# Kernel optimization log

Hardware: AMD Instinct MI355X
Metric: run time of the kernel (lower is better)

Reference implementation:

```python
import jax, jax.numpy as jnp
import numpy as np

B, C, D, H, W = 4, 64, 32, 64, 64
S, NH = 8, 4
HD = C // NH


def setup_inputs() -> dict:
    key = jax.random.key(0)
    ks = jax.random.split(key, 8)
    sc = 0.05
    return {
        "x": jax.random.normal(ks[0], (B, C, D, H, W), jnp.float32),
        "slot_init": jax.random.normal(ks[1], (1, C, S), jnp.float32),
        "slot_proj_w": jax.random.normal(ks[2], (C, C), jnp.float32) * sc,
        "slot_proj_b": jnp.zeros((C,), jnp.float32),
        "ln_g": jnp.ones((C,), jnp.float32),
        "ln_b": jnp.zeros((C,), jnp.float32),
        "in_proj_w": jax.random.normal(ks[3], (3 * C, C), jnp.float32) * sc,
        "in_proj_b": jnp.zeros((3 * C,), jnp.float32),
        "out_proj_w": jax.random.normal(ks[4], (C, C), jnp.float32) * sc,
        "out_proj_b": jnp.zeros((C,), jnp.float32),
        "feat_w": jax.random.normal(ks[5], (C, C), jnp.float32) * sc,
        "feat_b": jnp.zeros((C,), jnp.float32),
        "s2f_w": jax.random.normal(ks[6], (C, C), jnp.float32) * sc,
        "s2f_b": jnp.zeros((C,), jnp.float32),
    }


def _l2norm(v, axis):
    # F.normalize: v / max(||v||, eps)
    n = jnp.sqrt(jnp.sum(v * v, axis=axis, keepdims=True))
    return v / jnp.maximum(n, 1e-12)


def reference(x, slot_init, slot_proj_w, slot_proj_b, ln_g, ln_b,
              in_proj_w, in_proj_b, out_proj_w, out_proj_b,
              feat_w, feat_b, s2f_w, s2f_b):
    b, c, d, h, w = x.shape
    n = d * h * w
    x_flat = x.reshape(b, c, n)                                  # (b,c,N)
    slots = jnp.broadcast_to(slot_init, (b, c, S))               # (b,c,S)

    # ---- slot update: cosine-sim cross attention over N ----
    x_norm = _l2norm(x_flat, 1)
    slots_norm = _l2norm(slots, 1)
    sim = jnp.einsum('bcs,bcn->bsn', slots_norm, x_norm)         # (b,S,N)
    attn = jax.nn.softmax(sim, axis=2)
    updates = jnp.einsum('bcn,bsn->bsc', x_flat, attn)           # (b,S,c)
    slots_t = updates @ slot_proj_w.T + slot_proj_b              # (b,S,c)

    # ---- LayerNorm(channels) then tiny MHSA over S=8 slots ----
    mu = jnp.mean(slots_t, axis=-1, keepdims=True)
    var = jnp.mean((slots_t - mu) ** 2, axis=-1, keepdims=True)
    sn = (slots_t - mu) / jnp.sqrt(var + 1e-5) * ln_g + ln_b     # (b,S,c)

    qkv = sn @ in_proj_w.T + in_proj_b                           # (b,S,3c)
    q, k, v = jnp.split(qkv, 3, axis=-1)
    def heads(t):
        return t.reshape(b, S, NH, HD).transpose(0, 2, 1, 3)     # (b,H,S,hd)
    q, k, v = heads(q), heads(k), heads(v)
    scores = jnp.einsum('bhqd,bhkd->bhqk', q, k) / jnp.sqrt(jnp.float32(HD))
    a = jax.nn.softmax(scores, axis=-1)
    o = jnp.einsum('bhqk,bhkd->bhqd', a, v).transpose(0, 2, 1, 3).reshape(b, S, c)
    o = o @ out_proj_w.T + out_proj_b
    slots_t = slots_t + o                                        # (b,S,c)

    # ---- feature broadcast: 1x1x1 conv + slot->feature attention ----
    feat_flat = jnp.einsum('oc,bcn->bon', feat_w, x_flat) + feat_b[None, :, None]
    slots_feat = slots_t @ s2f_w.T + s2f_b                       # (b,S,c)
    sim2 = jnp.einsum('bsc,bcn->bsn', slots_feat, feat_flat)
    attn2 = jax.nn.softmax(sim2, axis=1)                         # softmax over slots
    out = jnp.einsum('bsc,bsn->bcn', slots_t, attn2)             # (b,c,N)
    return out.reshape(b, c, d, h, w) + x
```

## Files before the change

### kernel.cpp

```cpp
#include <hip/hip_runtime.h>
#include <hip/hip_bf16.h>

#define BB   4
#define CC   64
#define SS   8
#define NN   (32*64*64)
#define NH_  4
#define HD_  16
#define TN   256

typedef __attribute__((ext_vector_type(8))) short bf16x8;
typedef __attribute__((ext_vector_type(4))) float f32x4;

__device__ __forceinline__ unsigned short f2b(float f) {
    union { float f; unsigned u; } v; v.f = f;
    unsigned r = v.u + 0x7FFFu + ((v.u >> 16) & 1u);
    return (unsigned short)(r >> 16);
}

__global__ __launch_bounds__(256) void k_precomp(
    const float* __restrict__ slot_init,
    const float* __restrict__ s2fw, const float* __restrict__ s2fb,
    const float* __restrict__ fw, const float* __restrict__ fb,
    float* __restrict__ M, float* __restrict__ g0v,
    float* __restrict__ hv, float* __restrict__ h0,
    float* __restrict__ snT_ws)
{
    const int tid = threadIdx.x;
    if (blockIdx.x < 16) {
        const int cp = blockIdx.x*4 + (tid >> 6);
        const int c  = tid & 63;
        float acc = 0.f;
        #pragma unroll 8
        for (int o = 0; o < CC; ++o)
            acc += s2fw[o*CC + cp] * fw[o*CC + c];
        M[cp*CC + c] = acc;
    } else if (blockIdx.x == 16) {
        if (tid < 64) {
            float acc = 0.f;
            #pragma unroll 8
            for (int o = 0; o < CC; ++o) acc += s2fb[o] * fw[o*CC + tid];
            g0v[tid] = acc;
        } else if (tid < 128) {
            const int cp = tid - 64;
            float acc = 0.f;
            #pragma unroll 8
            for (int o = 0; o < CC; ++o) acc += s2fw[o*CC + cp] * fb[o];
            hv[cp] = acc;
        } else if (tid == 128) {
            float acc = 0.f;
            for (int o = 0; o < CC; ++o) acc += s2fb[o] * fb[o];
            *h0 = acc;
        }
    } else {
        __shared__ float nrm[SS];
        if (tid < 64) {
            const int s = tid & 7, ch = tid >> 3;
            float p = 0.f;
            #pragma unroll
            for (int j = 0; j < 8; ++j) {
                float v = slot_init[(ch*8 + j)*SS + s];
                p += v*v;
            }
            p += __shfl_xor(p, 8); p += __shfl_xor(p, 16); p += __shfl_xor(p, 32);
            if (tid < 8) nrm[s] = fmaxf(sqrtf(p), 1e-12f);
        }
        __syncthreads();
        for (int i = tid; i < SS*CC; i += 256) {
            const int s = i >> 6, c = i & 63;
            snT_ws[i] = slot_init[c*SS + s] / nrm[s];
        }
    }
}

__global__ __launch_bounds__(256, 4) void k_slots_attn(
    const float* __restrict__ x, const float* __restrict__ snT_ws,
    float* __restrict__ U_part, float* __restrict__ sume_part, int bpb)
{
    __shared__ short xt[CC * TN];
    __shared__ short et[9 * TN];
    __shared__ float snT[SS * CC];

    const int tid = threadIdx.x;
    const int b   = blockIdx.x / bpb;
    const int blk = blockIdx.x % bpb;

    if (tid < 64) *(int2*)&et[8*TN + tid*4] = make_int2(0, 0);
    if (tid < 128) *(float4*)&snT[tid*4] = *(const float4*)&snT_ws[tid*4];

    const int lane = tid & 63, wv = tid >> 6;
    const int n7 = tid & 7, nq3 = tid >> 3;
    f32x4 accU = {0.f, 0.f, 0.f, 0.f};
    float accS[SS];
    #pragma unroll
    for (int s = 0; s < SS; ++s) accS[s] = 0.f;

    const float* xb = x + (size_t)b * CC * NN;
    const int ntiles = NN / TN;

    for (int t = blk; t < ntiles; t += bpb) {
        const int n0 = t * TN;

        float xc[CC];
        #pragma unroll
        for (int c = 0; c < CC; ++c) xc[c] = xb[(size_t)c * NN + n0 + tid];

        __syncthreads();

        #pragma unroll
        for (int c = 0; c < CC; ++c)
            xt[c*TN + (((nq3 ^ (c & 7)) << 3) | n7)] = (short)f2b(xc[c]);

        {
            float ss = 0.f;
            float a[SS];
            #pragma unroll
            for (int s = 0; s < SS; ++s) a[s] = 0.f;
            #pragma unroll
            for (int c4 = 0; c4 < 16; ++c4) {
                const float xv0 = xc[c4*4+0], xv1 = xc[c4*4+1];
                const float xv2 = xc[c4*4+2], xv3 = xc[c4*4+3];
                ss += xv0*xv0 + xv1*xv1 + xv2*xv2 + xv3*xv3;
                #pragma unroll
                for (int s = 0; s < SS; ++s) {
                    const float4 g4 = *(const float4*)&snT[s*CC + c4*4];
                    a[s] += g4.x*xv0 + g4.y*xv1 + g4.z*xv2 + g4.w*xv3;
                }
            }
            const float invn = 1.f / fmaxf(sqrtf(ss), 1e-12f);
            #pragma unroll
            for (int s = 0; s < SS; ++s) {
                const float e = __expf(a[s] * invn);
                accS[s] += e;
                et[s*TN + (((nq3 ^ s) << 3) | n7)] = (short)f2b(e);
            }
        }
        __syncthreads();

        {
            const int ca  = (wv << 4) + (lane & 15);
            const int rbq = lane & 15;
            const int rb  = (rbq < 8) ? rbq : 8;
            const int p   = lane >> 4;
            #pragma unroll
            for (int k = 0; k < TN/32; ++k) {
                const int sa = ((((k << 2) + p) ^ (lane & 7)) << 3);
                bf16x8 af  = *(const bf16x8*)&xt[ca*TN + sa];
                bf16x8 bfr = *(const bf16x8*)&et[rb*TN + sa];
                accU = __builtin_amdgcn_mfma_f32_16x16x32_bf16(af, bfr, accU, 0, 0, 0);
            }
        }
    }
    __syncthreads();

    {
        const size_t base = ((size_t)(b*bpb + blk) * SS) * CC;
        if ((lane & 15) < SS) {
            const int s  = lane & 15;
            const int c0 = (wv << 4) + ((lane >> 4) << 2);
            #pragma unroll
            for (int r = 0; r < 4; ++r)
                U_part[base + s*CC + c0 + r] = accU[r];
        }
    }
    {
        float* red = (float*)xt;
        #pragma unroll
        for (int s = 0; s < SS; ++s) red[s*256 + tid] = accS[s];
        __syncthreads();
        const int s = tid >> 5, j = tid & 31;
        float v = 0.f;
        #pragma unroll
        for (int k = 0; k < 8; ++k) v += red[s*256 + j*8 + k];
        v += __shfl_xor(v, 1); v += __shfl_xor(v, 2); v += __shfl_xor(v, 4);
        v += __shfl_xor(v, 8); v += __shfl_xor(v, 16);
        if (j == 0) sume_part[(size_t)(b*bpb + blk)*SS + s] = v;
    }
}

__global__ __launch_bounds__(256) void k_reduce2(
    const float* __restrict__ U_part, const float* __restrict__ sume_part,
    float* __restrict__ upd_g, int bpb)
{
    __shared__ float part[4][64];
    __shared__ float lbuf[256];
    __shared__ float Lsh;
    const int tid = threadIdx.x;
    const int b = blockIdx.x >> 3, s = blockIdx.x & 7;
    const int c = tid & 63, kc = tid >> 6;
    const int cnt = bpb >> 2;

    float lv = 0.f;
    for (int k = tid; k < bpb; k += 256)
        lv += sume_part[(size_t)(b*bpb + k)*SS + s];
    lbuf[tid] = lv;

    float acc[8];
    #pragma unroll
    for (int j = 0; j < 8; ++j) acc[j] = 0.f;
    const float* base = U_part + ((size_t)(b*bpb + kc*cnt)*SS + s)*CC + c;
    for (int k = 0; k < cnt; k += 8) {
        #pragma unroll
        for (int j = 0; j < 8; ++j)
            acc[j] += base[(size_t)(k + j) * SS * CC];
    }
    part[kc][c] = ((acc[0]+acc[1]) + (acc[2]+acc[3]))
                + ((acc[4]+acc[5]) + (acc[6]+acc[7]));
    __syncthreads();

    if (tid < 128) lbuf[tid] += lbuf[tid + 128];
    __syncthreads();
    if (tid < 64) {
        float v = lbuf[tid] + lbuf[tid + 64];
        v += __shfl_xor(v, 1); v += __shfl_xor(v, 2); v += __shfl_xor(v, 4);
        v += __shfl_xor(v, 8); v += __shfl_xor(v, 16); v += __shfl_xor(v, 32);
        if (tid == 0) Lsh = v;
    }
    __syncthreads();

    if (tid < 64) {
        float u = part[0][c] + part[1][c] + part[2][c] + part[3][c];
        upd_g[((size_t)b*SS + s)*CC + c] = u / Lsh;
    }
}

__global__ __launch_bounds__(256) void k_slots_small(
    const float* __restrict__ upd_g,
    const float* __restrict__ spw, const float* __restrict__ spb,
    const float* __restrict__ lng, const float* __restrict__ lnb,
    const float* __restrict__ ipw, const float* __restrict__ ipb,
    const float* __restrict__ opw, const float* __restrict__ opb,
    const float* __restrict__ M, const float* __restrict__ g0v,
    const float* __restrict__ hv, const float* __restrict__ h0,
    float* __restrict__ st_out, float* __restrict__ g_out, float* __restrict__ h_out)
{
    __shared__ float upd[SS*CC];
    __shared__ float st [SS*CC];
    __shared__ float snb[SS*CC];
    __shared__ float qkv[SS*3*CC];
    __shared__ float ot [SS*CC];

    const int tid  = threadIdx.x;
    const int b    = blockIdx.x;
    const int c    = tid & 63;
    const int quad = tid >> 6;
    const int r0 = quad*2, r1 = r0 + 1;
    float wreg[CC];

    #pragma unroll
    for (int i = 0; i < 16; ++i)
        *(float4*)&wreg[i*4] = *(const float4*)(spw + c*CC + i*4);
    upd[r0*CC + c] = upd_g[(b*SS + r0)*CC + c];
    upd[r1*CC + c] = upd_g[(b*SS + r1)*CC + c];
    __syncthreads();

    {
        const float bias = spb[c];
        float a0 = bias, a1 = bias;
        #pragma unroll
        for (int i = 0; i < 16; ++i) {
            float4 u0 = *(const float4*)&upd[r0*CC + i*4];
            float4 u1 = *(const float4*)&upd[r1*CC + i*4];
            a0 += u0.x*wreg[i*4+0] + u0.y*wreg[i*4+1] + u0.z*wreg[i*4+2] + u0.w*wreg[i*4+3];
            a1 += u1.x*wreg[i*4+0] + u1.y*wreg[i*4+1] + u1.z*wreg[i*4+2] + u1.w*wreg[i*4+3];
        }
        st[r0*CC + c] = a0;
        st[r1*CC + c] = a1;
    }
    __syncthreads();

    {
        const int row = tid >> 5, l = tid & 31;
        float v0 = st[row*CC + l], v1 = st[row*CC + l + 32];
        float sum = v0 + v1;
        sum += __shfl_xor(sum, 1); sum += __shfl_xor(sum, 2); sum += __shfl_xor(sum, 4);
        sum += __shfl_xor(sum, 8); sum += __shfl_xor(sum, 16);
        const float mu = sum * (1.f/64.f);
        const float d0 = v0 - mu, d1 = v1 - mu;
        float vs = d0*d0 + d1*d1;
        vs += __shfl_xor(vs, 1); vs += __shfl_xor(vs, 2); vs += __shfl_xor(vs, 4);
        vs += __shfl_xor(vs, 8); vs += __shfl_xor(vs, 16);
        const float rstd = rsqrtf(vs * (1.f/64.f) + 1e-5f);
        snb[row*CC + l]      = d0 * rstd * lng[l]      + lnb[l];
        snb[row*CC + l + 32] = d1 * rstd * lng[l + 32] + lnb[l + 32];
    }
    __syncthreads();

    for (int m = 0; m < 3; ++m) {
        #pragma unroll
        for (int i = 0; i < 16; ++i)
            *(float4*)&wreg[i*4] = *(const float4*)(ipw + (size_t)(m*CC + c)*CC + i*4);
        const float bias = ipb[m*CC + c];
        float a0 = bias, a1 = bias;
        #pragma unroll
        for (int i = 0; i < 16; ++i) {
            float4 u0 = *(const float4*)&snb[r0*CC + i*4];
            float4 u1 = *(const float4*)&snb[r1*CC + i*4];
            a0 += u0.x*wreg[i*4+0] + u0.y*wreg[i*4+1] + u0.z*wreg[i*4+2] + u0.w*wreg[i*4+3];
            a1 += u1.x*wreg[i*4+0] + u1.y*wreg[i*4+1] + u1.z*wreg[i*4+2] + u1.w*wreg[i*4+3];
        }
        qkv[r0*3*CC + m*CC + c] = a0;
        qkv[r1*3*CC + m*CC + c] = a1;
    }
    __syncthreads();

    if (tid < NH_*SS) {
        const int h = tid >> 3, q = tid & 7;
        float qreg[HD_];
        #pragma unroll
        for (int i = 0; i < 4; ++i)
            *(float4*)&qreg[i*4] = *(const float4*)&qkv[q*3*CC + h*HD_ + i*4];
        float srow[SS];
        float mx = -1e30f;
        #pragma unroll
        for (int k = 0; k < SS; ++k) {
            float acc = 0.f;
            #pragma unroll
            for (int d = 0; d < HD_; ++d)
                acc += qreg[d] * qkv[k*3*CC + CC + h*HD_ + d];
            srow[k] = acc * 0.25f;
            mx = fmaxf(mx, srow[k]);
        }
        float l = 0.f;
        #pragma unroll
        for (int k = 0; k < SS; ++k) { srow[k] = __expf(srow[k] - mx); l += srow[k]; }
        const float inv = 1.f / l;
        float oreg[HD_];
        #pragma unroll
        for (int d = 0; d < HD_; ++d) oreg[d] = 0.f;
        #pragma unroll
        for (int k = 0; k < SS; ++k) {
            #pragma unroll
            for (int d = 0; d < HD_; ++d)
                oreg[d] += srow[k] * qkv[k*3*CC + 2*CC + h*HD_ + d];
        }
        #pragma unroll
        for (int d = 0; d < HD_; ++d)
            ot[q*CC + h*HD_ + d] = oreg[d] * inv;
    }
    __syncthreads();

    #pragma unroll
    for (int i = 0; i < 16; ++i)
        *(float4*)&wreg[i*4] = *(const float4*)(opw + c*CC + i*4);
    {
        const float bias = opb[c];
        float a0 = bias, a1 = bias;
        #pragma unroll
        for (int i = 0; i < 16; ++i) {
            float4 u0 = *(const float4*)&ot[r0*CC + i*4];
            float4 u1 = *(const float4*)&ot[r1*CC + i*4];
            a0 += u0.x*wreg[i*4+0] + u0.y*wreg[i*4+1] + u0.z*wreg[i*4+2] + u0.w*wreg[i*4+3];
            a1 += u1.x*wreg[i*4+0] + u1.y*wreg[i*4+1] + u1.z*wreg[i*4+2] + u1.w*wreg[i*4+3];
        }
        st[r0*CC + c] += a0;
        st[r1*CC + c] += a1;
    }
    __syncthreads();

    #pragma unroll 8
    for (int cp = 0; cp < CC; ++cp) wreg[cp] = M[cp*CC + c];
    {
        const float g0 = g0v[c];
        float a0 = g0, a1 = g0;
        #pragma unroll
        for (int i = 0; i < 16; ++i) {
            float4 s0 = *(const float4*)&st[r0*CC + i*4];
            float4 s1 = *(const float4*)&st[r1*CC + i*4];
            a0 += s0.x*wreg[i*4+0] + s0.y*wreg[i*4+1] + s0.z*wreg[i*4+2] + s0.w*wreg[i*4+3];
            a1 += s1.x*wreg[i*4+0] + s1.y*wreg[i*4+1] + s1.z*wreg[i*4+2] + s1.w*wreg[i*4+3];
        }
        g_out[(b*SS + r0)*CC + c] = a0;
        g_out[(b*SS + r1)*CC + c] = a1;
        st_out[(b*SS + r0)*CC + c] = st[r0*CC + c];
        st_out[(b*SS + r1)*CC + c] = st[r1*CC + c];
    }
    {
        const int row = tid >> 5, l = tid & 31;
        float pv = st[row*CC + l]*hv[l] + st[row*CC + l + 32]*hv[l + 32];
        pv += __shfl_xor(pv, 1); pv += __shfl_xor(pv, 2); pv += __shfl_xor(pv, 4);
        pv += __shfl_xor(pv, 8); pv += __shfl_xor(pv, 16);
        if (l == 0) h_out[b*SS + row] = pv + *h0;
    }
}

__global__ __launch_bounds__(256) void k_feat(
    const float* __restrict__ x,
    const float* __restrict__ st_g, const float* __restrict__ g_g,
    const float* __restrict__ h_g,
    float* __restrict__ out)
{
    __shared__ float stS[SS*CC];
    __shared__ float gS [SS*CC];
    __shared__ float hS [SS];

    const int tid = threadIdx.x;
    const int b  = blockIdx.x >> 9;
    const int n  = ((blockIdx.x & 511) << 8) + tid;

    for (int i = tid; i < SS*CC; i += 256) {
        stS[i] = st_g[b*SS*CC + i];
        gS[i]  = g_g [b*SS*CC + i];
    }
    if (tid < SS) hS[tid] = h_g[b*SS + tid];
    __syncthreads();

    const float* xb = x + (size_t)b * CC * NN + n;
    float xc[CC];
    #pragma unroll
    for (int c = 0; c < CC; ++c) xc[c] = xb[(size_t)c * NN];

    float a[SS];
    #pragma unroll
    for (int s = 0; s < SS; ++s) a[s] = hS[s];
    #pragma unroll
    for (int c4 = 0; c4 < CC/4; ++c4) {
        #pragma unroll
        for (int s = 0; s < SS; ++s) {
            float4 g4 = *(const float4*)(&gS[s*CC + c4*4]);
            a[s] += g4.x*xc[c4*4+0] + g4.y*xc[c4*4+1]
                  + g4.z*xc[c4*4+2] + g4.w*xc[c4*4+3];
        }
    }

    float m = a[0];
    #pragma unroll
    for (int s = 1; s < SS; ++s) m = fmaxf(m, a[s]);
    float l = 0.f;
    #pragma unroll
    for (int s = 0; s < SS; ++s) { a[s] = __expf(a[s] - m); l += a[s]; }
    const float inv = 1.f / l;

    float* ob = out + (size_t)b * CC * NN + n;
    #pragma unroll
    for (int c4 = 0; c4 < CC/4; ++c4) {
        float o0 = 0.f, o1 = 0.f, o2 = 0.f, o3 = 0.f;
        #pragma unroll
        for (int s = 0; s < SS; ++s) {
            float4 s4 = *(const float4*)(&stS[s*CC + c4*4]);
            o0 += s4.x * a[s]; o1 += s4.y * a[s];
            o2 += s4.z * a[s]; o3 += s4.w * a[s];
        }
        ob[(size_t)(c4*4+0) * NN] = o0 * inv + xc[c4*4+0];
        ob[(size_t)(c4*4+1) * NN] = o1 * inv + xc[c4*4+1];
        ob[(size_t)(c4*4+2) * NN] = o2 * inv + xc[c4*4+2];
        ob[(size_t)(c4*4+3) * NN] = o3 * inv + xc[c4*4+3];
    }
}

extern "C" void kernel_launch(void* const* d_in, const int* in_sizes, int n_in,
                              void* d_out, int out_size, void* d_ws, size_t ws_size,
                              hipStream_t stream) {
    const float* x         = (const float*)d_in[0];
    const float* slot_init = (const float*)d_in[1];
    const float* spw       = (const float*)d_in[2];
    const float* spb       = (const float*)d_in[3];
    const float* lng       = (const float*)d_in[4];
    const float* lnb       = (const float*)d_in[5];
    const float* ipw       = (const float*)d_in[6];
    const float* ipb       = (const float*)d_in[7];
    const float* opw       = (const float*)d_in[8];
    const float* opb       = (const float*)d_in[9];
    const float* fw        = (const float*)d_in[10];
    const float* fb        = (const float*)d_in[11];
    const float* s2fw      = (const float*)d_in[12];
    const float* s2fb      = (const float*)d_in[13];
    float* out = (float*)d_out;

    int bpb = 512;
    {
        size_t need = ((size_t)BB*bpb*SS*CC + (size_t)BB*bpb*SS
                       + 2048 + 4096 + 64 + 64 + 64 + 1024 + 2048 + 2048 + 32)
                      * sizeof(float);
        if (need > ws_size) bpb = 128;
    }

    float* w         = (float*)d_ws;
    float* U_part    = w;
    float* sume_part = U_part + (size_t)BB*bpb*SS*CC;
    float* upd_g     = sume_part + (size_t)BB*bpb*SS;
    float* Mm        = upd_g + 2048;
    float* g0v       = Mm + 4096;
    float* hv        = g0v + 64;
    float* h0        = hv + 64;
    float* snT_ws    = h0 + 64;
    float* st_out    = snT_ws + 1024;
    float* g_out     = st_out + 2048;
    float* h_out     = g_out + 2048;

    k_precomp<<<18, 256, 0, stream>>>(slot_init, s2fw, s2fb, fw, fb,
                                      Mm, g0v, hv, h0, snT_ws);
    k_slots_attn<<<BB * bpb, 256, 0, stream>>>(x, snT_ws, U_part, sume_part, bpb);
    k_reduce2<<<BB * SS, 256, 0, stream>>>(U_part, sume_part, upd_g, bpb);
    k_slots_small<<<BB, 256, 0, stream>>>(upd_g, spw, spb, lng, lnb,
                                          ipw, ipb, opw, opb, Mm, g0v, hv, h0,
                                          st_out, g_out, h_out);
    k_feat<<<BB * (NN/256), 256, 0, stream>>>(x, st_out, g_out, h_out, out);
}
```

Baseline: 136.1 us.

## Double-buffer x tiles into LDS with async global_load_lds in slot attention

```diff
diff --git a/kernel.cpp b/kernel.cpp
--- a/kernel.cpp
+++ b/kernel.cpp
@@ -7,7 +7,9 @@
 #define NN   (32*64*64)
 #define NH_  4
 #define HD_  16
-#define TN   256
+#define TA   128
+#define BPA  128
+#define NTB  8
 
 typedef __attribute__((ext_vector_type(8))) short bf16x8;
 typedef __attribute__((ext_vector_type(4))) float f32x4;
@@ -16,6 +18,12 @@
     union { float f; unsigned u; } v; v.f = f;
     unsigned r = v.u + 0x7FFFu + ((v.u >> 16) & 1u);
     return (unsigned short)(r >> 16);
+}
+__device__ __forceinline__ unsigned bfpack(float a, float b) {
+    union { float f; unsigned u; } x, y; x.f = a; y.f = b;
+    unsigned ra = (x.u + 0x7FFFu + ((x.u >> 16) & 1u)) >> 16;
+    unsigned rb = (y.u + 0x7FFFu + ((y.u >> 16) & 1u)) & 0xFFFF0000u;
+    return ra | rb;
 }
 
 __global__ __launch_bounds__(256) void k_precomp(
@@ -67,72 +75,91 @@
         }
         __syncthreads();
         for (int i = tid; i < SS*CC; i += 256) {
-            const int s = i >> 6, c = i & 63;
+            const int c = i >> 3, s = i & 7;
             snT_ws[i] = slot_init[c*SS + s] / nrm[s];
         }
     }
 }
 
-__global__ __launch_bounds__(256, 4) void k_slots_attn(
+__global__ __launch_bounds__(256) void k_slots_attn(
     const float* __restrict__ x, const float* __restrict__ snT_ws,
-    float* __restrict__ U_part, float* __restrict__ sume_part, int bpb)
+    float* __restrict__ U_part, float* __restrict__ sume_part)
 {
-    __shared__ short xt[CC * TN];
-    __shared__ short et[9 * TN];
-    __shared__ float snT[SS * CC];
+    __shared__ float xlds[2][CC * TA];
+    __shared__ short et[9 * TA];
+    __shared__ float snT[CC * SS];
+    __shared__ float red[2 * 9 * TA];
 
     const int tid = threadIdx.x;
-    const int b   = blockIdx.x / bpb;
-    const int blk = blockIdx.x % bpb;
-
-    if (tid < 64) *(int2*)&et[8*TN + tid*4] = make_int2(0, 0);
+    const int b   = blockIdx.x / BPA;
+    const int blk = blockIdx.x % BPA;
+    const int lane = tid & 63, wv = tid >> 6;
+    const int col = tid & 127, half = tid >> 7;
+
+    if (tid < 64) ((int*)&et[8*TA])[tid] = 0;
     if (tid < 128) *(float4*)&snT[tid*4] = *(const float4*)&snT_ws[tid*4];
 
-    const int lane = tid & 63, wv = tid >> 6;
-    const int n7 = tid & 7, nq3 = tid >> 3;
+    const float* xb = x + (size_t)b * CC * NN;
+
     f32x4 accU = {0.f, 0.f, 0.f, 0.f};
     float accS[SS];
     #pragma unroll
     for (int s = 0; s < SS; ++s) accS[s] = 0.f;
 
-    const float* xb = x + (size_t)b * CC * NN;
-    const int ntiles = NN / TN;
-
-    for (int t = blk; t < ntiles; t += bpb) {
-        const int n0 = t * TN;
-
-        float xc[CC];
-        #pragma unroll
-        for (int c = 0; c < CC; ++c) xc[c] = xb[(size_t)c * NN + n0 + tid];
-
-        __syncthreads();
-
-        #pragma unroll
-        for (int c = 0; c < CC; ++c)
-            xt[c*TN + (((nq3 ^ (c & 7)) << 3) | n7)] = (short)f2b(xc[c]);
+    #define STAGE(buf, t)                                                      \
+    {                                                                          \
+        const int n0_ = (t) * TA;                                              \
+        _Pragma("unroll")                                                      \
+        for (int k = 0; k < 8; ++k) {                                          \
+            const int c_  = (wv*8 + k)*2 + (lane >> 5);                        \
+            const int jg_ = (lane & 31) ^ (c_ & 7);                            \
+            const float* src_ = xb + (size_t)c_*NN + n0_ + jg_*4;              \
+            float* dst_ = &xlds[buf][(wv*8 + k)*256];                          \
+            __builtin_amdgcn_global_load_lds(                                  \
+                (const __attribute__((address_space(1))) void*)src_,           \
+                (__attribute__((address_space(3))) void*)dst_, 16, 0, 0);      \
+        }                                                                      \
+    }
+
+    int cur = 0;
+    STAGE(0, blk);
+    asm volatile("s_waitcnt vmcnt(0)" ::: "memory");
+    __syncthreads();
+
+    for (int tt = 0; tt < NTB; ++tt) {
+        if (tt + 1 < NTB) STAGE(cur ^ 1, blk + (tt+1)*BPA);
 
         {
+            const float* xl = &xlds[cur][0];
             float ss = 0.f;
             float a[SS];
             #pragma unroll
             for (int s = 0; s < SS; ++s) a[s] = 0.f;
             #pragma unroll
-            for (int c4 = 0; c4 < 16; ++c4) {
-                const float xv0 = xc[c4*4+0], xv1 = xc[c4*4+1];
-                const float xv2 = xc[c4*4+2], xv3 = xc[c4*4+3];
-                ss += xv0*xv0 + xv1*xv1 + xv2*xv2 + xv3*xv3;
-                #pragma unroll
-                for (int s = 0; s < SS; ++s) {
-                    const float4 g4 = *(const float4*)&snT[s*CC + c4*4];
-                    a[s] += g4.x*xv0 + g4.y*xv1 + g4.z*xv2 + g4.w*xv3;
-                }
+            for (int ci = 0; ci < 32; ++ci) {
+                const int c = half*32 + ci;
+                const float xv = xl[c*TA + (((col>>2) ^ (c&7)) << 2) + (col&3)];
+                ss += xv * xv;
+                const float4 g0 = *(const float4*)&snT[c*8];
+                const float4 g1 = *(const float4*)&snT[c*8 + 4];
+                a[0] += g0.x*xv; a[1] += g0.y*xv; a[2] += g0.z*xv; a[3] += g0.w*xv;
+                a[4] += g1.x*xv; a[5] += g1.y*xv; a[6] += g1.z*xv; a[7] += g1.w*xv;
             }
+            red[(half*9 + 8)*TA + col] = ss;
+            #pragma unroll
+            for (int s = 0; s < SS; ++s) red[(half*9 + s)*TA + col] = a[s];
+        }
+        __syncthreads();
+
+        if (tid < TA) {
+            const float ss = red[8*TA + tid] + red[(9+8)*TA + tid];
             const float invn = 1.f / fmaxf(sqrtf(ss), 1e-12f);
             #pragma unroll
             for (int s = 0; s < SS; ++s) {
-                const float e = __expf(a[s] * invn);
+                const float av = red[s*TA + tid] + red[(9+s)*TA + tid];
+                const float e = __expf(av * invn);
                 accS[s] += e;
-                et[s*TN + (((nq3 ^ s) << 3) | n7)] = (short)f2b(e);
+                et[s*TA + ((((tid>>3) ^ s) << 3) | (tid & 7))] = (short)f2b(e);
             }
         }
         __syncthreads();
@@ -143,18 +170,29 @@
             const int rb  = (rbq < 8) ? rbq : 8;
             const int p   = lane >> 4;
             #pragma unroll
-            for (int k = 0; k < TN/32; ++k) {
-                const int sa = ((((k << 2) + p) ^ (lane & 7)) << 3);
-                bf16x8 af  = *(const bf16x8*)&xt[ca*TN + sa];
-                bf16x8 bfr = *(const bf16x8*)&et[rb*TN + sa];
-                accU = __builtin_amdgcn_mfma_f32_16x16x32_bf16(af, bfr, accU, 0, 0, 0);
+            for (int kk = 0; kk < 4; ++kk) {
+                const int n8  = kk*32 + p*8;
+                const int sl0 = ((n8 >> 2)     ^ (ca & 7));
+                const int sl1 = (((n8 >> 2)+1) ^ (ca & 7));
+                const float4 f0 = *(const float4*)&xlds[cur][ca*TA + sl0*4];
+                const float4 f1 = *(const float4*)&xlds[cur][ca*TA + sl1*4];
+                union { unsigned u[4]; bf16x8 v; } ua;
+                ua.u[0] = bfpack(f0.x, f0.y);
+                ua.u[1] = bfpack(f0.z, f0.w);
+                ua.u[2] = bfpack(f1.x, f1.y);
+                ua.u[3] = bfpack(f1.z, f1.w);
+                const int slb = ((n8 >> 3) ^ (rb & 7));
+                const bf16x8 bfr = *(const bf16x8*)&et[rb*TA + slb*8];
+                accU = __builtin_amdgcn_mfma_f32_16x16x32_bf16(ua.v, bfr, accU, 0, 0, 0);
             }
         }
-    }
-    __syncthreads();
-
-    {
-        const size_t base = ((size_t)(b*bpb + blk) * SS) * CC;
+        asm volatile("s_waitcnt vmcnt(0)" ::: "memory");
+        __syncthreads();
+        cur ^= 1;
+    }
+
+    {
+        const size_t base = ((size_t)(b*BPA + blk) * SS) * CC;
         if ((lane & 15) < SS) {
             const int s  = lane & 15;
             const int c0 = (wv << 4) + ((lane >> 4) << 2);
@@ -163,19 +201,21 @@
                 U_part[base + s*CC + c0 + r] = accU[r];
         }
     }
-    {
-        float* red = (float*)xt;
-        #pragma unroll
-        for (int s = 0; s < SS; ++s) red[s*256 + tid] = accS[s];
-        __syncthreads();
+    if (tid < TA) {
+        #pragma unroll
+        for (int s = 0; s < SS; ++s) red[s*TA + tid] = accS[s];
+    }
+    __syncthreads();
+    {
         const int s = tid >> 5, j = tid & 31;
         float v = 0.f;
         #pragma unroll
-        for (int k = 0; k < 8; ++k) v += red[s*256 + j*8 + k];
+        for (int k = 0; k < 4; ++k) v += red[s*TA + j*4 + k];
         v += __shfl_xor(v, 1); v += __shfl_xor(v, 2); v += __shfl_xor(v, 4);
         v += __shfl_xor(v, 8); v += __shfl_xor(v, 16);
-        if (j == 0) sume_part[(size_t)(b*bpb + blk)*SS + s] = v;
-    }
+        if (j == 0) sume_part[(size_t)(b*BPA + blk)*SS + s] = v;
+    }
+    #undef STAGE
 }
 
 __global__ __launch_bounds__(256) void k_reduce2(
@@ -467,18 +507,10 @@
     const float* s2fb      = (const float*)d_in[13];
     float* out = (float*)d_out;
 
-    int bpb = 512;
-    {
-        size_t need = ((size_t)BB*bpb*SS*CC + (size_t)BB*bpb*SS
-                       + 2048 + 4096 + 64 + 64 + 64 + 1024 + 2048 + 2048 + 32)
-                      * sizeof(float);
-        if (need > ws_size) bpb = 128;
-    }
-
     float* w         = (float*)d_ws;
     float* U_part    = w;
-    float* sume_part = U_part + (size_t)BB*bpb*SS*CC;
-    float* upd_g     = sume_part + (size_t)BB*bpb*SS;
+    float* sume_part = U_part + (size_t)BB*BPA*SS*CC;
+    float* upd_g     = sume_part + (size_t)BB*BPA*SS;
     float* Mm        = upd_g + 2048;
     float* g0v       = Mm + 4096;
     float* hv        = g0v + 64;
@@ -490,8 +522,8 @@
 
     k_precomp<<<18, 256, 0, stream>>>(slot_init, s2fw, s2fb, fw, fb,
                                       Mm, g0v, hv, h0, snT_ws);
-    k_slots_attn<<<BB * bpb, 256, 0, stream>>>(x, snT_ws, U_part, sume_part, bpb);
-    k_reduce2<<<BB * SS, 256, 0, stream>>>(U_part, sume_part, upd_g, bpb);
+    k_slots_attn<<<BB * BPA, 256, 0, stream>>>(x, snT_ws, U_part, sume_part);
+    k_reduce2<<<BB * SS, 256, 0, stream>>>(U_part, sume_part, upd_g, BPA);
     k_slots_small<<<BB, 256, 0, stream>>>(upd_g, spw, spb, lng, lnb,
                                           ipw, ipb, opw, opb, Mm, g0v, hv, h0,
                                           st_out, g_out, h_out);
```

Result: faster. 127.2 us (-6.5%).
